# Kernel tuning notes

Hardware: AMD Instinct MI355X
Metric: run time of the kernel (lower is better)

Reference implementation:

```python
import jax, jax.numpy as jnp
import numpy as np
import math

B, SEQ, E, H, NB, NHYP = 4, 1024, 512, 8, 64, 6
V, HID, NC, ENC = 32000, 2048, 6, 6
DH = E // H


def _pos_encoding(n, e, dtype):
    pos = jnp.arange(n, dtype=dtype)[:, None]
    div = jnp.exp(-jnp.arange(0, e, 2, dtype=dtype) * (math.log(10000.0) / e))
    ang = pos * div  # [n, e/2]
    pe = jnp.zeros((n, e), dtype)
    pe = pe.at[:, 0::2].set(jnp.sin(ang))
    pe = pe.at[:, 1::2].set(jnp.cos(ang))
    return pe


def _layer_norm(x, g, b):
    m = x.mean(-1, keepdims=True)
    v = ((x - m) ** 2).mean(-1, keepdims=True)
    return (x - m) / jnp.sqrt(v + 1e-5) * g + b


def _lsh_attention(x, Wq, bq, Wv, bv, hyper):
    b, n, e = x.shape
    q = x @ Wq + bq
    v = x @ Wv + bv
    q4 = q.reshape(b, n, H, DH)  # [b,n,h,d]
    v4 = v.reshape(b, n, H, DH)
    # bucket hashing: append bias 1, project on hyperplanes, binarize, binary-encode
    aug = jnp.concatenate([q4, jnp.ones((b, n, H, 1), q.dtype)], axis=-1)
    proj = jnp.einsum('bnhe,ey->bnhy', aug, hyper)
    bits = (proj >= 0).astype(q.dtype)
    pows = (2 ** jnp.arange(NHYP)).astype(q.dtype)
    buckets = jnp.einsum('bnhy,y->bnh', bits, pows).astype(jnp.int32)
    bh = buckets.transpose(0, 2, 1)  # [b,h,n]
    qh = q4.transpose(0, 2, 1, 3)  # [b,h,n,d]
    vh = v4.transpose(0, 2, 1, 3)
    scores = jnp.einsum('bhnd,bhmd->bhnm', qh, qh) / math.sqrt(e)
    # torch code zeroes q rows at their OWN bucket and sums q_c @ q_c^T over all
    # NB buckets; that equals scores * (NB - 2 + [bucket_i == bucket_j]) exactly.
    same = bh[:, :, :, None] == bh[:, :, None, :]
    count = (NB - 2 + same.astype(jnp.int32)).astype(scores.dtype)
    attn = jax.nn.softmax(scores * count, axis=-1)
    out = jnp.einsum('bhnm,bhmd->bhnd', attn, vh)
    return out.transpose(0, 2, 1, 3).reshape(b, n, e)


def setup_inputs() -> dict:
    key = jax.random.key(0)
    ks = jax.random.split(key, 16)
    s = 0.02
    emb = jax.random.normal(ks[0], (V, E), jnp.float32) * s
    emb = emb.at[V - 1].set(0.0)  # padding_idx row
    return dict(
        inputs=jax.random.randint(ks[1], (B, SEQ), 0, V),
        emb=emb,
        gamma=jnp.ones((E,), jnp.float32),
        beta=jnp.zeros((E,), jnp.float32),
        Wq=jax.random.normal(ks[2], (E, E), jnp.float32) * s,
        bq=jnp.zeros((E,), jnp.float32),
        Wv=jax.random.normal(ks[3], (E, E), jnp.float32) * s,
        bv=jnp.zeros((E,), jnp.float32),
        hyper=jax.random.normal(ks[4], (DH + 1, NHYP), jnp.float32),
        W1=jax.random.normal(ks[5], (E, HID), jnp.float32) * s,
        b1=jnp.zeros((HID,), jnp.float32),
        W2=jax.random.normal(ks[6], (HID, E), jnp.float32) * s,
        b2=jnp.zeros((E,), jnp.float32),
        Wm=jax.random.normal(ks[7], (E * SEQ, NC), jnp.float32) * 0.002,
        bm=jnp.zeros((NC,), jnp.float32),
    )


def reference(inputs, emb, gamma, beta, Wq, bq, Wv, bv, hyper, W1, b1, W2, b2, Wm, bm):
    x = emb[inputs]  # [B, SEQ, E]
    x = x + _pos_encoding(x.shape[1], x.shape[2], x.dtype)
    for _ in range(ENC):  # shared weights across encoders
        a = _lsh_attention(x, Wq, bq, Wv, bv, hyper)
        x = _layer_norm(a, gamma, beta)
        x = jax.nn.relu(x @ W1 + b1) @ W2 + b2 + x
        x = _layer_norm(x, gamma, beta)
    x = x.reshape(x.shape[0], -1)
    return x @ Wm + bm  # [B, NC]
```

## Files before the change

kernel.cpp:

```cpp
#include <hip/hip_runtime.h>
#include <hip/hip_bf16.h>
#include <math.h>

#define B_    4
#define SEQ_  1024
#define E_    512
#define H_    8
#define DH_   64
#define NHYP_ 6
#define HID_  2048
#define NC_   6
#define ENC_  6
#define BH_   (B_*H_)
#define NTOK_ 4096
#define NCAT_ 1088

typedef __attribute__((ext_vector_type(8))) short short8;
typedef __attribute__((ext_vector_type(4))) float f32x4;

static __device__ __forceinline__ float wave_rsum(float v){
#pragma unroll
  for(int o=32;o;o>>=1) v += __shfl_down(v,o,64);
  return v;
}
static __device__ __forceinline__ ushort f2b(float v){
  __hip_bfloat16 h = __float2bfloat16(v);
  return *(ushort*)&h;
}
static __device__ __forceinline__ float b2f(ushort u){
  unsigned int x = ((unsigned int)u) << 16;
  return *(float*)&x;
}
static __device__ __forceinline__ void gload16(const void* g, void* l){
  __builtin_amdgcn_global_load_lds(
      (const __attribute__((address_space(1))) void*)g,
      (__attribute__((address_space(3))) void*)l,
      16, 0, 0);
}

__global__ void embed_pe_kernel(const int* __restrict__ inp, const float* __restrict__ emb,
                                float* __restrict__ x, ushort* __restrict__ xh){
  int row = blockIdx.x;
  int s = row & (SEQ_-1);
  int idx = inp[row];
  const float* er = emb + (size_t)idx*E_;
  float* xr = x + (size_t)row*E_;
  ushort* hr = xh + (size_t)row*E_;
  for(int c=threadIdx.x;c<E_;c+=blockDim.x){
    int i = c>>1;
    float div = expf(-(float)i * 0.0359778920780319646f);
    float ang = (float)s * div;
    float pe = (c&1) ? cosf(ang) : sinf(ang);
    float v = er[c] + pe;
    xr[c] = v;
    hr[c] = f2b(v);
  }
}

__global__ __launch_bounds__(256) void prep_kernel(
    const float* __restrict__ Wq, const float* __restrict__ Wv,
    const float* __restrict__ W1, const float* __restrict__ W2,
    const float* __restrict__ bq, const float* __restrict__ bv,
    const float* __restrict__ hyper,
    ushort* __restrict__ WcatT, ushort* __restrict__ W1T,
    ushort* __restrict__ W2T, float* __restrict__ bcat)
{
  int bid = blockIdx.x;
  if(bid < 2560){
    const float* W; ushort* Wt; int K, N, tile;
    if(bid < 256){       W=Wq; Wt=WcatT;                    K=512;  N=512;  tile=bid; }
    else if(bid < 512){  W=Wv; Wt=WcatT+(size_t)512*512;    K=512;  N=512;  tile=bid-256; }
    else if(bid < 1536){ W=W1; Wt=W1T;                      K=512;  N=2048; tile=bid-512; }
    else {               W=W2; Wt=W2T;                      K=2048; N=512;  tile=bid-1536; }
    int tpr = N >> 5;
    int n0 = (tile % tpr)*32, k0 = (tile / tpr)*32;
    __shared__ float T[32][33];
    int tx = threadIdx.x & 31, ty = threadIdx.x >> 5;
#pragma unroll
    for(int i=0;i<32;i+=8) T[ty+i][tx] = W[(size_t)(k0+ty+i)*N + n0+tx];
    __syncthreads();
#pragma unroll
    for(int i=0;i<32;i+=8)
      Wt[(size_t)(n0+ty+i)*K + k0+tx] = f2b(T[tx][ty+i]);
  } else if(bid < 2688){
    int t = (bid-2560)*256 + threadIdx.x;
    int c = t >> 9, k = t & 511;
    float s = 0.f;
    if(c < 48){
      int h = c/6, y = c%6;
      const float* wr = Wq + (size_t)k*E_ + h*DH_;
      for(int d=0;d<DH_;++d) s += wr[d]*hyper[d*NHYP_+y];
    }
    WcatT[(size_t)(1024+c)*E_ + k] = f2b(s);
  } else {
    int t = (bid-2688)*256 + threadIdx.x;
    if(t >= NCAT_) return;
    float v;
    if(t < 512) v = bq[t];
    else if(t < 1024) v = bv[t-512];
    else if(t < 1072){
      int c = t - 1024, h = c/6, y = c%6;
      float s = hyper[DH_*NHYP_ + y];
      for(int d=0;d<DH_;++d) s += bq[h*DH_+d]*hyper[d*NHYP_+y];
      v = s;
    } else v = 0.f;
    bcat[t] = v;
  }
}

template<int BM, int BN, int EPI>
__global__ __launch_bounds__(256) void gemm_mfma(
    const ushort* __restrict__ A, const ushort* __restrict__ Bt,
    const float* __restrict__ bias, const float* __restrict__ res,
    void* __restrict__ C0, void* __restrict__ C1, void* __restrict__ C2,
    void* __restrict__ C3, int M, int N, int K)
{
  constexpr int MI = BM/32, NI = BN/32;
  constexpr int ACH = BM/32, BCH = BN/32;
  __shared__ ushort As[2][BM*64];
  __shared__ ushort Bs[2][BN*64];
  __shared__ float epi[64*49];
  int tid = threadIdx.x;
  int w = tid>>6, lane = tid&63, g = lane>>4, li = lane&15;
  int wr = w>>1, wc = w&1;
  int bm = blockIdx.y*BM, bn = blockIdx.x*BN;
  int kz = blockIdx.z;
  int kcnt = K / (int)gridDim.z;
  int kbase = kz * kcnt;
  int NK = kcnt >> 6;

  f32x4 acc[MI][NI] = {};

  auto issue = [&](int ks, int pb){
    int k0 = kbase + ks*64;
#pragma unroll
    for(int it=0; it<ACH; ++it){
      int c = it*256 + tid; int r = c>>3; int kq = ((c&7)^(r&7))*8;
      gload16(&A[(size_t)(bm+r)*K + k0 + kq], &As[pb][it*2048 + w*512]);
    }
#pragma unroll
    for(int it=0; it<BCH; ++it){
      int c = it*256 + tid; int r = c>>3; int kq = ((c&7)^(r&7))*8;
      gload16(&Bt[(size_t)(bn+r)*K + k0 + kq], &Bs[pb][it*2048 + w*512]);
    }
  };

  issue(0, 0);
  __syncthreads();
  for(int ks=0; ks<NK; ++ks){
    if(ks+1 < NK) issue(ks+1, (ks+1)&1);
    int pb = ks&1;
#pragma unroll
    for(int kc=0; kc<2; ++kc){
      short8 af[MI], bf[NI];
#pragma unroll
      for(int mi=0;mi<MI;++mi)
        af[mi] = *(const short8*)&As[pb][(wr*(BM/2)+mi*16+li)*64 + (((kc*4+g)^(li&7))*8)];
#pragma unroll
      for(int ni=0;ni<NI;++ni)
        bf[ni] = *(const short8*)&Bs[pb][(wc*(BN/2)+ni*16+li)*64 + (((kc*4+g)^(li&7))*8)];
#pragma unroll
      for(int mi=0;mi<MI;++mi)
#pragma unroll
        for(int ni=0;ni<NI;++ni)
          acc[mi][ni] = __builtin_amdgcn_mfma_f32_16x16x32_bf16(af[mi], bf[ni], acc[mi][ni], 0,0,0);
    }
    __syncthreads();
  }

  if(EPI==5){
    if(bn < 512){
      int h = bn >> 6;
#pragma unroll
      for(int mi=0;mi<MI;++mi){
        int rbase = bm + wr*(BM/2) + mi*16 + g*4;
        float q2s[4] = {0.f,0.f,0.f,0.f};
#pragma unroll
        for(int ni=0;ni<NI;++ni){
          int cc = bn + wc*(BN/2) + ni*16 + li;
          float bv = bias[cc];
          int d = cc & 63;
#pragma unroll
          for(int j=0;j<4;++j){
            float vvf = acc[mi][ni][j] + bv;
            ushort ub = f2b(vvf);
            int r = rbase + j; int b = r>>10, n = r&1023;
            ((ushort*)C1)[(((size_t)(b*8+h))*1024 + n)*64 + d] = ub;
            float f = b2f(ub);
            q2s[j] += f*f;
          }
        }
#pragma unroll
        for(int j=0;j<4;++j){
#pragma unroll
          for(int o=8;o;o>>=1) q2s[j] += __shfl_xor(q2s[j], o, 64);
        }
        if(li==0){
#pragma unroll
          for(int j=0;j<4;++j)
            epi[(wr*(BM/2)+mi*16+g*4+j)*2 + wc] = q2s[j];
        }
      }
      __syncthreads();
      if(tid < 64){
        int r = bm + tid; int b = r>>10, n = r&1023;
        ((float*)C3)[((size_t)(b*8+h))*1024 + n] = epi[tid*2] + epi[tid*2+1];
      }
    } else if(bn < 1024){
#pragma unroll
      for(int mi=0;mi<MI;++mi){
        int rbase = bm + wr*(BM/2) + mi*16 + g*4;
        int b = rbase>>10, n = rbase&1023;
#pragma unroll
        for(int ni=0;ni<NI;++ni){
          int cc = bn + wc*(BN/2) + ni*16 + li;
          float bv = bias[cc];
          int cl = cc - 512; int h = cl>>6, d = cl&63;
          ushort4 pk;
          pk.x = f2b(acc[mi][ni][0]+bv); pk.y = f2b(acc[mi][ni][1]+bv);
          pk.z = f2b(acc[mi][ni][2]+bv); pk.w = f2b(acc[mi][ni][3]+bv);
          *(ushort4*)&((ushort*)C2)[(((size_t)(b*8+h))*64 + d)*1024 + n] = pk;
        }
      }
    } else {
#pragma unroll
      for(int mi=0;mi<MI;++mi){
        int rloc = wr*(BM/2) + mi*16 + g*4;
#pragma unroll
        for(int ni=0;ni<NI;++ni){
          int c = wc*(BN/2) + ni*16 + li;
          if(c < 48){
            float bv = bias[1024 + c];
#pragma unroll
            for(int j=0;j<4;++j)
              epi[(rloc+j)*49 + c] = acc[mi][ni][j] + bv;
          }
        }
      }
      __syncthreads();
      if(tid < 64){
        int r = bm + tid; int b = r>>10, n = r&1023;
#pragma unroll
        for(int h=0;h<8;++h){
          int bk = 0;
#pragma unroll
          for(int y=0;y<NHYP_;++y)
            bk |= (epi[tid*49 + h*NHYP_ + y] >= 0.0f) ? (1<<y) : 0;
          ((int*)C0)[((size_t)(b*8+h))*1024 + n] = bk;
        }
      }
    }
    return;
  }

#pragma unroll
  for(int mi=0;mi<MI;++mi){
    int rbase = bm + wr*(BM/2) + mi*16 + g*4;
#pragma unroll
    for(int ni=0;ni<NI;++ni){
      int cc = bn + wc*(BN/2) + ni*16 + li;
      float bv = (EPI==6) ? 0.0f : bias[cc];
      float vv[4];
#pragma unroll
      for(int j=0;j<4;++j) vv[j] = acc[mi][ni][j] + bv;
      if(EPI==1){
#pragma unroll
        for(int j=0;j<4;++j) ((ushort*)C0)[(size_t)(rbase+j)*N + cc] = f2b(fmaxf(vv[j],0.0f));
      } else if(EPI==6){
        float* dst = (float*)C0 + (size_t)kz*M*N;
#pragma unroll
        for(int j=0;j<4;++j) dst[(size_t)(rbase+j)*N + cc] = vv[j];
      } else if(EPI==2){
#pragma unroll
        for(int j=0;j<4;++j){
          size_t o = (size_t)(rbase+j)*N + cc;
          ((float*)C0)[o] = vv[j] + res[o];
        }
      } else {
#pragma unroll
        for(int j=0;j<4;++j) ((float*)C0)[(size_t)(rbase+j)*N + cc] = vv[j];
      }
    }
  }
}

__global__ __launch_bounds__(256) void attn_mfma_kernel(
    const ushort* __restrict__ Qh,
    const ushort* __restrict__ Vt,
    const int* __restrict__ buckets,
    const float* __restrict__ qn2,
    float* __restrict__ Op,
    float* __restrict__ Sp)
{
  int bid = blockIdx.x;
  int bh   = bid & 31;
  int half = (bid >> 5) & 1;
  int qt   = bid >> 6;
  int b = bh >> 3, h = bh & 7;
  int tid = threadIdx.x;
  int w = tid >> 6, lane = tid & 63;
  int g = lane >> 4, li = lane & 15;

  __shared__ ushort Ks[2][64*64];
  __shared__ ushort Vs[2][64*64];
  __shared__ ushort Ps[64*68];
  __shared__ int bks[2][64];
  __shared__ int bqs[64];
  __shared__ float mred[4];

  const ushort* Qbase = Qh + (size_t)bh*SEQ_*DH_;
  const ushort* Vbase = Vt + (size_t)bh*DH_*SEQ_;
  const int* Bb = buckets + bh*SEQ_;
  const float* qn = qn2 + bh*SEQ_;
  int q0 = qt*64;
  int kt0 = half*8;

  auto issue = [&](int kt, int pb){
    int j0 = kt*64;
#pragma unroll
    for(int it=0; it<2; ++it){
      int c = it*256 + tid; int r = c>>3; int ks = ((c&7)^(r&7))*8;
      gload16(&Qbase[(size_t)(j0+r)*DH_ + ks], &Ks[pb][it*2048 + w*512]);
      gload16(&Vbase[(size_t)r*SEQ_ + j0 + ks], &Vs[pb][it*2048 + w*512]);
    }
    if(tid < 16) gload16(&Bb[j0 + tid*4], &bks[pb][0]);
  };

  issue(kt0, 0);
  short8 qa[2];
  int qrow = q0 + w*16 + li;
#pragma unroll
  for(int kc=0; kc<2; ++kc)
    qa[kc] = *(const short8*)&Qbase[(size_t)qrow*DH_ + kc*32 + g*8];
  if(tid < 64) bqs[tid] = Bb[q0 + tid];

  float mx = 0.f;
  for(int i=tid;i<SEQ_;i+=256) mx = fmaxf(mx, qn[i]);
#pragma unroll
  for(int o=32;o;o>>=1) mx = fmaxf(mx, __shfl_xor(mx, o, 64));
  if(lane==0) mred[w] = mx;
  __syncthreads();
  float maxn = sqrtf(fmaxf(fmaxf(mred[0],mred[1]), fmaxf(mred[2],mred[3])));

  const float invsq = 0.04419417382415922f;
  const float LOG2E = 1.4426950408889634f;
  const float c62l = invsq * 62.0f * LOG2E;
  const float c63l = invsq * 63.0f * LOG2E;
  float nM2[4];
#pragma unroll
  for(int i=0;i<4;++i){
    float Mrow = invsq*63.0f * sqrtf(qn[q0 + w*16 + g*4 + i]) * maxn + 1.0f;
    nM2[i] = -Mrow * LOG2E;
  }

  f32x4 acc_o[4] = {};
  float psum[4] = {0.f,0.f,0.f,0.f};

  for(int t=0; t<8; ++t){
    int kt = kt0 + t;
    if(t < 7) issue(kt+1, (t+1)&1);
    int pb = t&1;

    f32x4 accs[4];
    __builtin_amdgcn_s_setprio(1);
#pragma unroll
    for(int nt=0; nt<4; ++nt){
      f32x4 z = {};
#pragma unroll
      for(int kc=0; kc<2; ++kc){
        short8 kb = *(const short8*)&Ks[pb][(nt*16+li)*64 + (((kc*4+g)^(li&7))*8)];
        z = __builtin_amdgcn_mfma_f32_16x16x32_bf16(qa[kc], kb, z, 0,0,0);
      }
      accs[nt] = z;
    }
    __builtin_amdgcn_s_setprio(0);
    int bkc[4];
#pragma unroll
    for(int nt=0;nt<4;++nt) bkc[nt] = bks[pb][nt*16 + li];

#pragma unroll
    for(int i=0;i<4;++i){
      int rloc = w*16 + g*4 + i;
      int bq = bqs[rloc];
      float rs = 0.f;
#pragma unroll
      for(int nt=0;nt<4;++nt){
        float cl = (bkc[nt] == bq) ? c63l : c62l;
        float e = exp2f(fmaf(accs[nt][i], cl, nM2[i]));
        rs += e;
        Ps[rloc*68 + nt*16 + li] = f2b(e);
      }
      psum[i] += rs;
    }
    __builtin_amdgcn_s_setprio(1);
#pragma unroll
    for(int dt=0; dt<4; ++dt){
      f32x4 z = acc_o[dt];
#pragma unroll
      for(int kc=0; kc<2; ++kc){
        short8 pa = *(const short8*)&Ps[(w*16+li)*68 + kc*32 + g*8];
        short8 vb = *(const short8*)&Vs[pb][(dt*16+li)*64 + (((kc*4+g)^(li&7))*8)];
        z = __builtin_amdgcn_mfma_f32_16x16x32_bf16(pa, vb, z, 0,0,0);
      }
      acc_o[dt] = z;
    }
    __builtin_amdgcn_s_setprio(0);
    __syncthreads();
  }
#pragma unroll
  for(int i=0;i<4;++i){
#pragma unroll
    for(int o=8;o;o>>=1) psum[i] += __shfl_xor(psum[i], o, 64);
  }
  float* obase = Op + (size_t)half*NTOK_*E_
               + ((size_t)(b*SEQ_ + q0 + w*16 + g*4))*E_ + h*DH_;
#pragma unroll
  for(int i=0;i<4;++i){
#pragma unroll
    for(int dt=0;dt<4;++dt)
      obase[(size_t)i*E_ + dt*16 + li] = acc_o[dt][i];
  }
  if(li == 0){
    float* sp = Sp + (size_t)half*BH_*SEQ_ + (size_t)bh*SEQ_ + q0 + w*16 + g*4;
#pragma unroll
    for(int i=0;i<4;++i) sp[i] = psum[i];
  }
}

__global__ __launch_bounds__(256) void combine_ln(
    const float* __restrict__ Op, const float* __restrict__ Sp,
    const float* __restrict__ g, const float* __restrict__ bb,
    float* __restrict__ outp, ushort* __restrict__ oh){
  int row = blockIdx.x*4 + (threadIdx.x>>6);
  int lane = threadIdx.x & 63;
  int b = row >> 10, n = row & 1023;
  int h = lane >> 3;
  size_t sidx = (size_t)(b*8+h)*SEQ_ + n;
  float ps = Sp[sidx] + Sp[(size_t)BH_*SEQ_ + sidx];
  float inv0 = 1.0f / fmaxf(ps, 1e-35f);
  const float4* o1 = (const float4*)(Op + (size_t)row*E_) + lane*2;
  const float4* o2 = (const float4*)(Op + (size_t)NTOK_*E_ + (size_t)row*E_) + lane*2;
  float4 v0 = o1[0], v1 = o1[1], u0 = o2[0], u1 = o2[1];
  v0.x=(v0.x+u0.x)*inv0; v0.y=(v0.y+u0.y)*inv0; v0.z=(v0.z+u0.z)*inv0; v0.w=(v0.w+u0.w)*inv0;
  v1.x=(v1.x+u1.x)*inv0; v1.y=(v1.y+u1.y)*inv0; v1.z=(v1.z+u1.z)*inv0; v1.w=(v1.w+u1.w)*inv0;
  float s  = v0.x+v0.y+v0.z+v0.w + v1.x+v1.y+v1.z+v1.w;
  float s2 = v0.x*v0.x+v0.y*v0.y+v0.z*v0.z+v0.w*v0.w
           + v1.x*v1.x+v1.y*v1.y+v1.z*v1.z+v1.w*v1.w;
#pragma unroll
  for(int o=32;o;o>>=1){ s += __shfl_xor(s,o,64); s2 += __shfl_xor(s2,o,64); }
  float mean = s*(1.0f/E_);
  float var  = s2*(1.0f/E_) - mean*mean;
  float inv = rsqrtf(var + 1e-5f);
  const float4* g4 = (const float4*)(g) + lane*2;
  const float4* b4 = (const float4*)(bb) + lane*2;
  float4 g0 = g4[0], g1 = g4[1], b0 = b4[0], b1 = b4[1];
  float4 y0, y1;
  y0.x=(v0.x-mean)*inv*g0.x+b0.x; y0.y=(v0.y-mean)*inv*g0.y+b0.y;
  y0.z=(v0.z-mean)*inv*g0.z+b0.z; y0.w=(v0.w-mean)*inv*g0.w+b0.w;
  y1.x=(v1.x-mean)*inv*g1.x+b1.x; y1.y=(v1.y-mean)*inv*g1.y+b1.y;
  y1.z=(v1.z-mean)*inv*g1.z+b1.z; y1.w=(v1.w-mean)*inv*g1.w+b1.w;
  float4* orow = (float4*)(outp + (size_t)row*E_) + lane*2;
  orow[0] = y0; orow[1] = y1;
  ushort hs[8];
  hs[0]=f2b(y0.x); hs[1]=f2b(y0.y); hs[2]=f2b(y0.z); hs[3]=f2b(y0.w);
  hs[4]=f2b(y1.x); hs[5]=f2b(y1.y); hs[6]=f2b(y1.z); hs[7]=f2b(y1.w);
  *(uint4*)&oh[(size_t)row*E_ + lane*8] = *(uint4*)hs;
}

__global__ __launch_bounds__(256) void ln2_kernel(
    const float* __restrict__ P, const float* __restrict__ b2,
    const float* __restrict__ Xres, const float* __restrict__ g,
    const float* __restrict__ bb, float* __restrict__ outp,
    ushort* __restrict__ oh){
  int row = blockIdx.x*4 + (threadIdx.x>>6);
  int lane = threadIdx.x & 63;
  const float4* p0 = (const float4*)(P + (size_t)row*E_) + lane*2;
  const float4* p1 = (const float4*)(P + (size_t)NTOK_*E_ + (size_t)row*E_) + lane*2;
  const float4* xr = (const float4*)(Xres + (size_t)row*E_) + lane*2;
  const float4* c4 = (const float4*)(b2) + lane*2;
  float4 v0 = p0[0], v1 = p0[1], u0 = p1[0], u1 = p1[1];
  float4 x0 = xr[0], x1 = xr[1], cb0 = c4[0], cb1 = c4[1];
  v0.x += u0.x + cb0.x + x0.x; v0.y += u0.y + cb0.y + x0.y;
  v0.z += u0.z + cb0.z + x0.z; v0.w += u0.w + cb0.w + x0.w;
  v1.x += u1.x + cb1.x + x1.x; v1.y += u1.y + cb1.y + x1.y;
  v1.z += u1.z + cb1.z + x1.z; v1.w += u1.w + cb1.w + x1.w;
  float s  = v0.x+v0.y+v0.z+v0.w + v1.x+v1.y+v1.z+v1.w;
  float s2 = v0.x*v0.x+v0.y*v0.y+v0.z*v0.z+v0.w*v0.w
           + v1.x*v1.x+v1.y*v1.y+v1.z*v1.z+v1.w*v1.w;
#pragma unroll
  for(int o=32;o;o>>=1){ s += __shfl_xor(s,o,64); s2 += __shfl_xor(s2,o,64); }
  float mean = s*(1.0f/E_);
  float var  = s2*(1.0f/E_) - mean*mean;
  float inv = rsqrtf(var + 1e-5f);
  const float4* g4 = (const float4*)(g) + lane*2;
  const float4* b4 = (const float4*)(bb) + lane*2;
  float4 g0 = g4[0], g1 = g4[1], b0 = b4[0], b1 = b4[1];
  float4 y0, y1;
  y0.x=(v0.x-mean)*inv*g0.x+b0.x; y0.y=(v0.y-mean)*inv*g0.y+b0.y;
  y0.z=(v0.z-mean)*inv*g0.z+b0.z; y0.w=(v0.w-mean)*inv*g0.w+b0.w;
  y1.x=(v1.x-mean)*inv*g1.x+b1.x; y1.y=(v1.y-mean)*inv*g1.y+b1.y;
  y1.z=(v1.z-mean)*inv*g1.z+b1.z; y1.w=(v1.w-mean)*inv*g1.w+b1.w;
  float4* orow = (float4*)(outp + (size_t)row*E_) + lane*2;
  orow[0] = y0; orow[1] = y1;
  ushort hs[8];
  hs[0]=f2b(y0.x); hs[1]=f2b(y0.y); hs[2]=f2b(y0.z); hs[3]=f2b(y0.w);
  hs[4]=f2b(y1.x); hs[5]=f2b(y1.y); hs[6]=f2b(y1.z); hs[7]=f2b(y1.w);
  *(uint4*)&oh[(size_t)row*E_ + lane*8] = *(uint4*)hs;
}

__global__ void final_partial(const float* __restrict__ x, const float* __restrict__ Wm,
                              float* __restrict__ part){
  int b  = blockIdx.x >> 7;
  int ch = blockIdx.x & 127;
  const float* xb = x + (size_t)b*SEQ_*E_;
  int k0 = ch*4096;
  float acc[NC_] = {};
  for(int k=k0+threadIdx.x; k<k0+4096; k+=256){
    float xv = xb[k];
    const float* wrow = Wm + (size_t)k*NC_;
#pragma unroll
    for(int c=0;c<NC_;++c) acc[c] += xv*wrow[c];
  }
#pragma unroll
  for(int c=0;c<NC_;++c) acc[c] = wave_rsum(acc[c]);
  __shared__ float r[4][NC_];
  int w = threadIdx.x>>6, lane = threadIdx.x&63;
  if(lane==0){
#pragma unroll
    for(int c=0;c<NC_;++c) r[w][c] = acc[c];
  }
  __syncthreads();
  if(threadIdx.x==0){
#pragma unroll
    for(int c=0;c<NC_;++c)
      part[(size_t)blockIdx.x*NC_ + c] = r[0][c]+r[1][c]+r[2][c]+r[3][c];
  }
}

__global__ void final_reduce(const float* __restrict__ part, const float* __restrict__ bm,
                             float* __restrict__ out){
  int t = threadIdx.x;
  if(t >= B_*NC_) return;
  int b = t / NC_, c = t % NC_;
  float s = bm[c];
  for(int i=0;i<128;++i) s += part[(size_t)(b*128+i)*NC_ + c];
  out[t] = s;
}

extern "C" void kernel_launch(void* const* d_in, const int* in_sizes, int n_in,
                              void* d_out, int out_size, void* d_ws, size_t ws_size,
                              hipStream_t stream){
  const int*   inp   = (const int*)d_in[0];
  const float* emb   = (const float*)d_in[1];
  const float* gamma = (const float*)d_in[2];
  const float* beta  = (const float*)d_in[3];
  const float* Wq    = (const float*)d_in[4];
  const float* bq    = (const float*)d_in[5];
  const float* Wv    = (const float*)d_in[6];
  const float* bv    = (const float*)d_in[7];
  const float* hyper = (const float*)d_in[8];
  const float* W1    = (const float*)d_in[9];
  const float* b1    = (const float*)d_in[10];
  const float* W2    = (const float*)d_in[11];
  const float* b2    = (const float*)d_in[12];
  const float* Wm    = (const float*)d_in[13];
  const float* bm    = (const float*)d_in[14];
  float* out = (float*)d_out;

  char* ws = (char*)d_ws;
  size_t off = 0;
  auto alloc = [&](size_t bytes)->void*{
    void* p = ws + off; off += (bytes + 255) & ~(size_t)255; return p;
  };
  const size_t NTOK = (size_t)B_*SEQ_;
  float*  X    = (float*)alloc(NTOK*E_*sizeof(float));
  float*  Op   = (float*)alloc((size_t)2*NTOK*E_*sizeof(float));
  float*  Sp   = (float*)alloc((size_t)2*BH_*SEQ_*sizeof(float));
  ushort* Xh   = (ushort*)alloc(NTOK*E_*sizeof(ushort));
  ushort* Hh   = (ushort*)alloc(NTOK*HID_*sizeof(ushort));
  int*    Bk   = (int*)  alloc((size_t)BH_*SEQ_*sizeof(int));
  float*  Qn2  = (float*)alloc((size_t)BH_*SEQ_*sizeof(float));
  float*  Pp   = (float*)alloc((size_t)B_*128*NC_*sizeof(float));
  ushort* Qh   = (ushort*)alloc((size_t)BH_*SEQ_*DH_*sizeof(ushort));
  ushort* Vt   = (ushort*)alloc((size_t)BH_*DH_*SEQ_*sizeof(ushort));
  ushort* WcatT= (ushort*)alloc((size_t)NCAT_*E_*sizeof(ushort));
  ushort* W1T  = (ushort*)alloc((size_t)HID_*E_*sizeof(ushort));
  ushort* W2T  = (ushort*)alloc((size_t)E_*HID_*sizeof(ushort));
  float*  bcat = (float*)alloc(NCAT_*sizeof(float));
  (void)ws_size; (void)in_sizes; (void)n_in; (void)out_size;

  prep_kernel<<<2693, 256, 0, stream>>>(Wq, Wv, W1, W2, bq, bv, hyper,
                                        WcatT, W1T, W2T, bcat);
  embed_pe_kernel<<<B_*SEQ_, 256, 0, stream>>>(inp, emb, X, Xh);

  dim3 gQV(NCAT_/64, (B_*SEQ_)/64);
  dim3 gF1(HID_/128, (B_*SEQ_)/128);
  dim3 gF2(E_/64,    (B_*SEQ_)/64, 2);
  for(int l=0;l<ENC_;++l){
    gemm_mfma<64,64,5><<<gQV, 256, 0, stream>>>(Xh, WcatT, bcat, nullptr, Bk, Qh, Vt, Qn2, B_*SEQ_, NCAT_, E_);
    attn_mfma_kernel<<<BH_*32, 256, 0, stream>>>(Qh, Vt, Bk, Qn2, Op, Sp);
    combine_ln<<<B_*SEQ_/4, 256, 0, stream>>>(Op, Sp, gamma, beta, X, Xh);
    gemm_mfma<128,128,1><<<gF1, 256, 0, stream>>>(Xh, W1T, b1, nullptr, Hh, nullptr, nullptr, nullptr, B_*SEQ_, HID_, E_);
    gemm_mfma<64,64,6><<<gF2, 256, 0, stream>>>(Hh, W2T, b2, nullptr, Op, nullptr, nullptr, nullptr, B_*SEQ_, E_, HID_);
    ln2_kernel<<<B_*SEQ_/4, 256, 0, stream>>>(Op, b2, X, gamma, beta, X, Xh);
  }
  final_partial<<<B_*128, 256, 0, stream>>>(X, Wm, Pp);
  final_reduce<<<1, 32, 0, stream>>>(Pp, bm, out);
}
```

Measured before the change: 606.7 us.

## Drop split-K attention, compute per-head max norm via atomicMax in QV GEMM

The attention kernel no longer splits the key range into two halves. Each block now walks all 16 key tiles and normalizes its output in place, so the separate partial-sum combine step becomes a plain layernorm. The per-head maximum query norm, which every attention block used to recompute by scanning 1024 values, is now reduced once in the QV GEMM epilogue with atomicMax into a small buffer. That buffer is zeroed by the embed kernel and the layernorm kernel. The grid is halved to 512 blocks, which lowers parallelism but removes a 2x partial-output write and read.

```diff
diff --git a/kernel.cpp b/kernel.cpp
--- a/kernel.cpp
+++ b/kernel.cpp
@@ -39,8 +39,10 @@
 }
 
 __global__ void embed_pe_kernel(const int* __restrict__ inp, const float* __restrict__ emb,
-                                float* __restrict__ x, ushort* __restrict__ xh){
+                                float* __restrict__ x, ushort* __restrict__ xh,
+                                unsigned int* __restrict__ MaxN){
   int row = blockIdx.x;
+  if(blockIdx.x==0 && threadIdx.x<32) MaxN[threadIdx.x] = 0u;
   int s = row & (SEQ_-1);
   int idx = inp[row];
   const float* er = emb + (size_t)idx*E_;
@@ -204,7 +206,15 @@
       __syncthreads();
       if(tid < 64){
         int r = bm + tid; int b = r>>10, n = r&1023;
-        ((float*)C3)[((size_t)(b*8+h))*1024 + n] = epi[tid*2] + epi[tid*2+1];
+        float q2 = epi[tid*2] + epi[tid*2+1];
+        ((float*)C3)[((size_t)(b*8+h))*1024 + n] = q2;
+        float m = q2;
+#pragma unroll
+        for(int o=32;o;o>>=1) m = fmaxf(m, __shfl_xor(m, o, 64));
+        if(tid==0){
+          int bh = (bm>>10)*8 + h;
+          atomicMax((unsigned int*)res + bh, __float_as_uint(m));
+        }
       }
     } else if(bn < 1024){
 #pragma unroll
@@ -289,13 +299,12 @@
     const ushort* __restrict__ Vt,
     const int* __restrict__ buckets,
     const float* __restrict__ qn2,
-    float* __restrict__ Op,
-    float* __restrict__ Sp)
+    const unsigned int* __restrict__ MaxN,
+    float* __restrict__ outp)
 {
   int bid = blockIdx.x;
-  int bh   = bid & 31;
-  int half = (bid >> 5) & 1;
-  int qt   = bid >> 6;
+  int bh = bid & 31;
+  int qt = bid >> 5;
   int b = bh >> 3, h = bh & 7;
   int tid = threadIdx.x;
   int w = tid >> 6, lane = tid & 63;
@@ -306,14 +315,12 @@
   __shared__ ushort Ps[64*68];
   __shared__ int bks[2][64];
   __shared__ int bqs[64];
-  __shared__ float mred[4];
 
   const ushort* Qbase = Qh + (size_t)bh*SEQ_*DH_;
   const ushort* Vbase = Vt + (size_t)bh*DH_*SEQ_;
   const int* Bb = buckets + bh*SEQ_;
   const float* qn = qn2 + bh*SEQ_;
   int q0 = qt*64;
-  int kt0 = half*8;
 
   auto issue = [&](int kt, int pb){
     int j0 = kt*64;
@@ -326,7 +333,7 @@
     if(tid < 16) gload16(&Bb[j0 + tid*4], &bks[pb][0]);
   };
 
-  issue(kt0, 0);
+  issue(0, 0);
   short8 qa[2];
   int qrow = q0 + w*16 + li;
 #pragma unroll
@@ -334,13 +341,7 @@
     qa[kc] = *(const short8*)&Qbase[(size_t)qrow*DH_ + kc*32 + g*8];
   if(tid < 64) bqs[tid] = Bb[q0 + tid];
 
-  float mx = 0.f;
-  for(int i=tid;i<SEQ_;i+=256) mx = fmaxf(mx, qn[i]);
-#pragma unroll
-  for(int o=32;o;o>>=1) mx = fmaxf(mx, __shfl_xor(mx, o, 64));
-  if(lane==0) mred[w] = mx;
-  __syncthreads();
-  float maxn = sqrtf(fmaxf(fmaxf(mred[0],mred[1]), fmaxf(mred[2],mred[3])));
+  float maxn = sqrtf(__uint_as_float(MaxN[bh]));
 
   const float invsq = 0.04419417382415922f;
   const float LOG2E = 1.4426950408889634f;
@@ -352,14 +353,14 @@
     float Mrow = invsq*63.0f * sqrtf(qn[q0 + w*16 + g*4 + i]) * maxn + 1.0f;
     nM2[i] = -Mrow * LOG2E;
   }
+  __syncthreads();
 
   f32x4 acc_o[4] = {};
   float psum[4] = {0.f,0.f,0.f,0.f};
 
-  for(int t=0; t<8; ++t){
-    int kt = kt0 + t;
-    if(t < 7) issue(kt+1, (t+1)&1);
-    int pb = t&1;
+  for(int kt=0; kt<16; ++kt){
+    if(kt < 15) issue(kt+1, (kt+1)&1);
+    int pb = kt&1;
 
     f32x4 accs[4];
     __builtin_amdgcn_s_setprio(1);
@@ -412,37 +413,25 @@
 #pragma unroll
     for(int o=8;o;o>>=1) psum[i] += __shfl_xor(psum[i], o, 64);
   }
-  float* obase = Op + (size_t)half*NTOK_*E_
-               + ((size_t)(b*SEQ_ + q0 + w*16 + g*4))*E_ + h*DH_;
+  float* obase = outp + ((size_t)(b*SEQ_ + q0 + w*16 + g*4))*E_ + h*DH_;
 #pragma unroll
   for(int i=0;i<4;++i){
+    float inv = 1.0f / fmaxf(psum[i], 1e-35f);
 #pragma unroll
     for(int dt=0;dt<4;++dt)
-      obase[(size_t)i*E_ + dt*16 + li] = acc_o[dt][i];
-  }
-  if(li == 0){
-    float* sp = Sp + (size_t)half*BH_*SEQ_ + (size_t)bh*SEQ_ + q0 + w*16 + g*4;
-#pragma unroll
-    for(int i=0;i<4;++i) sp[i] = psum[i];
-  }
-}
-
-__global__ __launch_bounds__(256) void combine_ln(
-    const float* __restrict__ Op, const float* __restrict__ Sp,
-    const float* __restrict__ g, const float* __restrict__ bb,
-    float* __restrict__ outp, ushort* __restrict__ oh){
+      obase[(size_t)i*E_ + dt*16 + li] = acc_o[dt][i] * inv;
+  }
+}
+
+__global__ __launch_bounds__(256) void ln_kernel(
+    const float* __restrict__ in, const float* __restrict__ g,
+    const float* __restrict__ bb, float* __restrict__ outp,
+    ushort* __restrict__ oh, unsigned int* __restrict__ MaxN){
+  if(blockIdx.x==0 && threadIdx.x<32) MaxN[threadIdx.x] = 0u;
   int row = blockIdx.x*4 + (threadIdx.x>>6);
   int lane = threadIdx.x & 63;
-  int b = row >> 10, n = row & 1023;
-  int h = lane >> 3;
-  size_t sidx = (size_t)(b*8+h)*SEQ_ + n;
-  float ps = Sp[sidx] + Sp[(size_t)BH_*SEQ_ + sidx];
-  float inv0 = 1.0f / fmaxf(ps, 1e-35f);
-  const float4* o1 = (const float4*)(Op + (size_t)row*E_) + lane*2;
-  const float4* o2 = (const float4*)(Op + (size_t)NTOK_*E_ + (size_t)row*E_) + lane*2;
-  float4 v0 = o1[0], v1 = o1[1], u0 = o2[0], u1 = o2[1];
-  v0.x=(v0.x+u0.x)*inv0; v0.y=(v0.y+u0.y)*inv0; v0.z=(v0.z+u0.z)*inv0; v0.w=(v0.w+u0.w)*inv0;
-  v1.x=(v1.x+u1.x)*inv0; v1.y=(v1.y+u1.y)*inv0; v1.z=(v1.z+u1.z)*inv0; v1.w=(v1.w+u1.w)*inv0;
+  const float4* xr = (const float4*)(in + (size_t)row*E_);
+  float4 v0 = xr[lane*2], v1 = xr[lane*2+1];
   float s  = v0.x+v0.y+v0.z+v0.w + v1.x+v1.y+v1.z+v1.w;
   float s2 = v0.x*v0.x+v0.y*v0.y+v0.z*v0.z+v0.w*v0.w
            + v1.x*v1.x+v1.y*v1.y+v1.z*v1.z+v1.w*v1.w;
@@ -574,12 +563,13 @@
   };
   const size_t NTOK = (size_t)B_*SEQ_;
   float*  X    = (float*)alloc(NTOK*E_*sizeof(float));
+  float*  A    = (float*)alloc(NTOK*E_*sizeof(float));
   float*  Op   = (float*)alloc((size_t)2*NTOK*E_*sizeof(float));
-  float*  Sp   = (float*)alloc((size_t)2*BH_*SEQ_*sizeof(float));
   ushort* Xh   = (ushort*)alloc(NTOK*E_*sizeof(ushort));
   ushort* Hh   = (ushort*)alloc(NTOK*HID_*sizeof(ushort));
   int*    Bk   = (int*)  alloc((size_t)BH_*SEQ_*sizeof(int));
   float*  Qn2  = (float*)alloc((size_t)BH_*SEQ_*sizeof(float));
+  unsigned int* MaxN = (unsigned int*)alloc(32*sizeof(unsigned int));
   float*  Pp   = (float*)alloc((size_t)B_*128*NC_*sizeof(float));
   ushort* Qh   = (ushort*)alloc((size_t)BH_*SEQ_*DH_*sizeof(ushort));
   ushort* Vt   = (ushort*)alloc((size_t)BH_*DH_*SEQ_*sizeof(ushort));
@@ -591,15 +581,16 @@
 
   prep_kernel<<<2693, 256, 0, stream>>>(Wq, Wv, W1, W2, bq, bv, hyper,
                                         WcatT, W1T, W2T, bcat);
-  embed_pe_kernel<<<B_*SEQ_, 256, 0, stream>>>(inp, emb, X, Xh);
+  embed_pe_kernel<<<B_*SEQ_, 256, 0, stream>>>(inp, emb, X, Xh, MaxN);
 
   dim3 gQV(NCAT_/64, (B_*SEQ_)/64);
   dim3 gF1(HID_/128, (B_*SEQ_)/128);
   dim3 gF2(E_/64,    (B_*SEQ_)/64, 2);
   for(int l=0;l<ENC_;++l){
-    gemm_mfma<64,64,5><<<gQV, 256, 0, stream>>>(Xh, WcatT, bcat, nullptr, Bk, Qh, Vt, Qn2, B_*SEQ_, NCAT_, E_);
-    attn_mfma_kernel<<<BH_*32, 256, 0, stream>>>(Qh, Vt, Bk, Qn2, Op, Sp);
-    combine_ln<<<B_*SEQ_/4, 256, 0, stream>>>(Op, Sp, gamma, beta, X, Xh);
+    gemm_mfma<64,64,5><<<gQV, 256, 0, stream>>>(Xh, WcatT, bcat, (const float*)MaxN,
+                                                Bk, Qh, Vt, Qn2, B_*SEQ_, NCAT_, E_);
+    attn_mfma_kernel<<<BH_*16, 256, 0, stream>>>(Qh, Vt, Bk, Qn2, MaxN, A);
+    ln_kernel<<<B_*SEQ_/4, 256, 0, stream>>>(A, gamma, beta, X, Xh, MaxN);
     gemm_mfma<128,128,1><<<gF1, 256, 0, stream>>>(Xh, W1T, b1, nullptr, Hh, nullptr, nullptr, nullptr, B_*SEQ_, HID_, E_);
     gemm_mfma<64,64,6><<<gF2, 256, 0, stream>>>(Hh, W2T, b2, nullptr, Op, nullptr, nullptr, nullptr, B_*SEQ_, E_, HID_);
     ln2_kernel<<<B_*SEQ_/4, 256, 0, stream>>>(Op, b2, X, gamma, beta, X, Xh);
```

Result: no change. 596.5 us, median of 2 (-1.7%).
